# Optimization experiments

Hardware: AMD Instinct MI355X
Metric: run time of the kernel (lower is better)

Reference implementation:

```python
import jax, jax.numpy as jnp
import numpy as np

B, BT = 64, 16              # total crops, true batch (B = 4 crops * BT)
IMG, PATCH, C = 224, 16, 3
EMB, HEADS, DEPTH = 192, 3, 12
MLP = 4 * EMB
NPATCH = (IMG // PATCH) ** 2      # 196
NTOK = NPATCH + 1                 # 197 (cls + patches)
NSLICE = 16
SAT_H, SAT_DK = 8, 32             # ScaledDotProductAttention(d_model=192, d_k=d_v=32, h=8)
SAT_D = SAT_H * SAT_DK            # 256


def setup_inputs() -> dict:
    ks = jax.random.split(jax.random.key(0), 16)
    n = lambda i, shape: jax.random.normal(ks[i], shape, jnp.float32) * 0.02
    z = lambda *s: jnp.zeros(s, jnp.float32)
    o = lambda *s: jnp.ones(s, jnp.float32)
    return {
        "x": jax.random.normal(ks[0], (B, C, IMG, IMG), jnp.float32),
        "x_g_norm": jax.random.uniform(ks[1], (BT, 1, IMG, IMG), dtype=jnp.float32),
        "per_li": jnp.linspace(1.0 / 16.0, 15.0 / 16.0, 15, dtype=jnp.float32),
        "per_li_var": jnp.linspace(0.01, 0.15, 15, dtype=jnp.float32),
        "patch_w": n(2, (EMB, C, PATCH, PATCH)), "patch_b": z(EMB),
        "cls_token": n(3, (1, 1, EMB)), "pos_embed": n(4, (1, NTOK, EMB)),
        "eleva_embed": n(5, (NSLICE, EMB)), "eleva_var_embed": n(6, (NSLICE, EMB)),
        "sat_wq": n(7, (EMB, SAT_D)), "sat_bq": z(SAT_D),
        "sat_wk": n(8, (EMB, SAT_D)), "sat_bk": z(SAT_D),
        "sat_wv": n(9, (EMB, SAT_D)), "sat_bv": z(SAT_D),
        "sat_wo": n(10, (SAT_D, EMB)), "sat_bo": z(EMB),
        "ln1_w": o(DEPTH, EMB), "ln1_b": z(DEPTH, EMB),
        "qkv_w": n(11, (DEPTH, EMB, 3 * EMB)),
        "proj_w": n(12, (DEPTH, EMB, EMB)), "proj_b": z(DEPTH, EMB),
        "ln2_w": o(DEPTH, EMB), "ln2_b": z(DEPTH, EMB),
        "fc1_w": n(13, (DEPTH, EMB, MLP)), "fc1_b": z(DEPTH, MLP),
        "fc2_w": n(14, (DEPTH, MLP, EMB)), "fc2_b": z(DEPTH, EMB),
        "lnf_w": o(EMB), "lnf_b": z(EMB),
    }


def _ln(x, w, b, eps=1e-5):
    mu = x.mean(-1, keepdims=True)
    var = ((x - mu) ** 2).mean(-1, keepdims=True)
    return (x - mu) * jax.lax.rsqrt(var + eps) * w + b


def reference(x, x_g_norm, per_li, per_li_var, patch_w, patch_b, cls_token, pos_embed,
              eleva_embed, eleva_var_embed, sat_wq, sat_bq, sat_wk, sat_bk, sat_wv, sat_bv,
              sat_wo, sat_bo, ln1_w, ln1_b, qkv_w, proj_w, proj_b, ln2_w, ln2_b,
              fc1_w, fc1_b, fc2_w, fc2_b, lnf_w, lnf_b):
    Btot, Bt = x.shape[0], x_g_norm.shape[0]
    # --- PatchEmbed (Conv2d patch=stride=16) ---
    feat = jax.lax.conv_general_dilated(
        x, patch_w, (PATCH, PATCH), 'VALID',
        dimension_numbers=('NCHW', 'OIHW', 'NCHW')) + patch_b[None, :, None, None]
    tok = feat.reshape(Btot, EMB, NPATCH).transpose(0, 2, 1)          # [B,196,E]
    tok = jnp.concatenate([jnp.broadcast_to(cls_token, (Btot, 1, EMB)), tok], 1)
    tok = tok + pos_embed                                             # [B,197,E]
    # --- elevation indices (bisect_left on per-sample mean / unbiased var) ---
    flat = x_g_norm.reshape(Bt, -1)
    idx = jnp.searchsorted(per_li, flat.mean(-1), side='left')
    vidx = jnp.searchsorted(per_li_var, jnp.var(flat, axis=-1, ddof=1), side='left')
    crops = Btot // Bt
    ele = jnp.tile(eleva_embed[idx], (crops, 1))                      # [B,E]
    vele = jnp.tile(eleva_var_embed[vidx], (crops, 1))                # [B,E]
    # --- tiny 3-token attention per (sample, token), batched ---
    at = jnp.stack([tok,
                    jnp.broadcast_to(ele[:, None, :], tok.shape),
                    jnp.broadcast_to(vele[:, None, :], tok.shape)], axis=2)  # [B,T,3,E]
    M = Btot * NTOK
    at = at.reshape(M, 3, EMB)
    q = (at @ sat_wq + sat_bq).reshape(M, 3, SAT_H, SAT_DK).transpose(0, 2, 1, 3)
    k = (at @ sat_wk + sat_bk).reshape(M, 3, SAT_H, SAT_DK).transpose(0, 2, 1, 3)
    v = (at @ sat_wv + sat_bv).reshape(M, 3, SAT_H, SAT_DK).transpose(0, 2, 1, 3)
    att = jax.nn.softmax(jnp.einsum('mhqd,mhkd->mhqk', q, k) / np.sqrt(SAT_DK).astype(np.float32), axis=-1)
    o = jnp.einsum('mhqk,mhkd->mhqd', att, v).transpose(0, 2, 1, 3).reshape(M, 3, SAT_D)
    o = o @ sat_wo + sat_bo                                           # [M,3,E]
    tok = o.sum(1).reshape(Btot, NTOK, EMB)   # token' + eleEm' + elevarEm'
    # --- standard ViT blocks ---
    hd = EMB // HEADS
    scale = hd ** -0.5
    for i in range(DEPTH):
        h = _ln(tok, ln1_w[i], ln1_b[i])
        qkv = (h @ qkv_w[i]).reshape(Btot, NTOK, 3, HEADS, hd).transpose(2, 0, 3, 1, 4)
        a = jax.nn.softmax(jnp.einsum('bhqd,bhkd->bhqk', qkv[0], qkv[1]) * scale, axis=-1)
        h = jnp.einsum('bhqk,bhkd->bhqd', a, qkv[2]).transpose(0, 2, 1, 3).reshape(Btot, NTOK, EMB)
        tok = tok + h @ proj_w[i] + proj_b[i]
        h2 = _ln(tok, ln2_w[i], ln2_b[i])
        h2 = jax.nn.gelu(h2 @ fc1_w[i] + fc1_b[i], approximate=False)
        tok = tok + h2 @ fc2_w[i] + fc2_b[i]
    tok = _ln(tok, lnf_w, lnf_b)
    return tok[:, 0]
```

## Files before the change

### kernel.cpp

```cpp
#include <hip/hip_runtime.h>
#include <hip/hip_bf16.h>
#include <math.h>

#define NB 64
#define NBT 16
#define IMG 224
#define CIN 3
#define EMB 192
#define NHEADS 3
#define DEPTH 12
#define MLPD (4*EMB)
#define NPATCH 196
#define NTOK 197
#define M_TOK (NB*NTOK)
#define M_PATCH (NB*NPATCH)
#define SAT_H 8
#define SAT_DK 32
#define SAT_D 256
#define KPV 232

typedef __attribute__((ext_vector_type(8))) short bf16x8;
typedef __attribute__((ext_vector_type(4))) float f32x4;
typedef __hip_bfloat16 bf16;

__device__ __forceinline__ float bf2f(ushort u) { return __uint_as_float(((unsigned)u) << 16); }
__device__ __forceinline__ ushort f2bf(float f) {
    bf16 h = __float2bfloat16(f);
    return *reinterpret_cast<ushort*>(&h);
}

__global__ __launch_bounds__(256) void stats1_kernel(const float* __restrict__ xg, double* __restrict__ part)
{
    int j = blockIdx.x, s = blockIdx.y;
    const float4* src = (const float4*)(xg + (size_t)s*(IMG*IMG)) + (size_t)j*784;
    double ls = 0.0, lq = 0.0;
    for (int i = threadIdx.x; i < 784; i += 256) {
        float4 v = src[i];
        double a = v.x, b = v.y, c = v.z, d = v.w;
        ls += a+b+c+d;
        lq += a*a + b*b + c*c + d*d;
    }
    __shared__ double ssum[256], ssq[256];
    ssum[threadIdx.x] = ls; ssq[threadIdx.x] = lq;
    __syncthreads();
    for (int st = 128; st > 0; st >>= 1) {
        if (threadIdx.x < st) { ssum[threadIdx.x] += ssum[threadIdx.x+st]; ssq[threadIdx.x] += ssq[threadIdx.x+st]; }
        __syncthreads();
    }
    if (threadIdx.x == 0) {
        part[(size_t)(s*16 + j)*2]     = ssum[0];
        part[(size_t)(s*16 + j)*2 + 1] = ssq[0];
    }
}

__global__ __launch_bounds__(64) void stats2_kernel(const double* __restrict__ part,
    const float* __restrict__ per_li, const float* __restrict__ per_li_var, int* __restrict__ idx_out)
{
    int s = blockIdx.x;
    if (threadIdx.x != 0) return;
    double sum = 0.0, sq = 0.0;
    for (int j = 0; j < 16; j++) { sum += part[(size_t)(s*16+j)*2]; sq += part[(size_t)(s*16+j)*2+1]; }
    double n = (double)(IMG*IMG);
    double mean = sum / n;
    double var  = (sq - n*mean*mean) / (n - 1.0);
    int i1 = 0, i2 = 0;
    for (int j = 0; j < 15; j++) {
        if ((double)per_li[j] < mean) i1++;
        if ((double)per_li_var[j] < var) i2++;
    }
    idx_out[s] = i1; idx_out[16 + s] = i2;
}

__global__ __launch_bounds__(256) void transpose_cast_kernel(const float* __restrict__ in,
    bf16* __restrict__ out, int K, int N)
{
    in  += (size_t)blockIdx.z*K*N;
    out += (size_t)blockIdx.z*N*K;
    __shared__ float t[32][33];
    int k0 = blockIdx.y*32, n0 = blockIdx.x*32;
    int tx = threadIdx.x & 31, ty = threadIdx.x >> 5;
    #pragma unroll
    for (int i = 0; i < 4; i++) {
        int k = ty + i*8;
        t[k][tx] = in[(size_t)(k0+k)*N + n0 + tx];
    }
    __syncthreads();
    #pragma unroll
    for (int i = 0; i < 4; i++) {
        int n = ty + i*8;
        out[(size_t)(n0+n)*K + k0 + tx] = __float2bfloat16(t[tx][n]);
    }
}

__global__ __launch_bounds__(256) void cast_kernel(const float* __restrict__ in, bf16* __restrict__ out, int n)
{
    int i = blockIdx.x*256 + threadIdx.x;
    if (i < n) out[i] = __float2bfloat16(in[i]);
}

__global__ __launch_bounds__(256) void concat3_kernel(const float* __restrict__ a,
    const float* __restrict__ b, const float* __restrict__ c, float* __restrict__ o)
{
    int i = blockIdx.x*256 + threadIdx.x;
    if (i < 256) o[i] = a[i];
    else if (i < 512) o[i] = b[i-256];
    else if (i < 768) o[i] = c[i-512];
}

__global__ __launch_bounds__(256) void im2col_kernel(const float* __restrict__ x, bf16* __restrict__ out)
{
    int e = blockIdx.x*256 + threadIdx.x;
    if (e >= M_PATCH*768) return;
    int row = e / 768, col = e % 768;
    int b = row / NPATCH, p = row % NPATCH;
    int py = p / 14, px = p % 14;
    int c = col >> 8, r8 = col & 255;
    int i = r8 >> 4, j = r8 & 15;
    out[e] = __float2bfloat16(x[(((size_t)b*CIN + c)*IMG + py*16 + i)*IMG + px*16 + j]);
}

__global__ void cls_kernel(const float* __restrict__ cls, const float* __restrict__ pos, bf16* __restrict__ tokb)
{
    int i = blockIdx.x*256 + threadIdx.x;
    if (i >= NB*EMB) return;
    int b = i / EMB, e = i % EMB;
    tokb[(size_t)(b*NTOK)*EMB + e] = __float2bfloat16(cls[e] + pos[e]);
}

template<int EPI, bool OBF>
__global__ __launch_bounds__(256) void mfma_gemm(
    const bf16* __restrict__ A, const bf16* __restrict__ Wt,
    const float* __restrict__ bias, const float* __restrict__ aux,
    void* __restrict__ Cv, int M, int N, int K, int ldc, float bias_scale)
{
    __shared__ bf16 As[64][72];
    __shared__ bf16 Bs[64][72];
    int tid = threadIdx.x;
    int wave = tid >> 6, lane = tid & 63;
    int wm = wave >> 1, wn = wave & 1;
    int m0 = blockIdx.y*64, n0 = blockIdx.x*64;
    f32x4 acc[2][2] = {};
    int sr = tid >> 3, sc = (tid & 7) * 8;

    for (int k0 = 0; k0 < K; k0 += 64) {
        #pragma unroll
        for (int it = 0; it < 2; it++) {
            int r = sr + it*32;
            *(uint4*)&As[r][sc] = *(const uint4*)(A  + (size_t)(m0 + r)*K + k0 + sc);
            *(uint4*)&Bs[r][sc] = *(const uint4*)(Wt + (size_t)(n0 + r)*K + k0 + sc);
        }
        __syncthreads();
        #pragma unroll
        for (int ks = 0; ks < 2; ks++) {
            int ko = ks*32 + (lane >> 4)*8;
            bf16x8 af[2], bfr[2];
            #pragma unroll
            for (int mi = 0; mi < 2; mi++) af[mi]  = *(const bf16x8*)&As[wm*32 + mi*16 + (lane & 15)][ko];
            #pragma unroll
            for (int ni = 0; ni < 2; ni++) bfr[ni] = *(const bf16x8*)&Bs[wn*32 + ni*16 + (lane & 15)][ko];
            #pragma unroll
            for (int mi = 0; mi < 2; mi++)
                #pragma unroll
                for (int ni = 0; ni < 2; ni++)
                    acc[mi][ni] = __builtin_amdgcn_mfma_f32_16x16x32_bf16(af[mi], bfr[ni], acc[mi][ni], 0, 0, 0);
        }
        __syncthreads();
    }
    #pragma unroll
    for (int mi = 0; mi < 2; mi++) {
        #pragma unroll
        for (int ni = 0; ni < 2; ni++) {
            int rbase = m0 + wm*32 + mi*16 + (lane >> 4)*4;
            int col   = n0 + wn*32 + ni*16 + (lane & 15);
            #pragma unroll
            for (int r = 0; r < 4; r++) {
                int row = rbase + r;
                float v = acc[mi][ni][r];
                if constexpr (EPI == 4) {
                    int b_ = row / NPATCH, p = row % NPATCH;
                    ((bf16*)Cv)[(size_t)(b_*NTOK + 1 + p)*EMB + col] =
                        __float2bfloat16(v + bias[col] + aux[(size_t)(1+p)*EMB + col]);
                } else if constexpr (EPI == 5) {
                    int hd = row >> 6, d = row & 63;
                    int bb = col / NTOK, t = col - bb*NTOK;
                    ((bf16*)Cv)[((size_t)((bb*3 + hd)*64 + d))*KPV + t] = __float2bfloat16(v);
                } else {
                    if constexpr (EPI == 1) v += bias[col]*bias_scale;
                    if constexpr (EPI == 2) v = ((float*)Cv)[(size_t)row*ldc + col] + v + bias[col];
                    if constexpr (EPI == 3) { v += bias[col]; v = 0.5f*v*(1.0f + erff(v*0.70710678118654752f)); }
                    if constexpr (OBF) ((bf16*)Cv)[(size_t)row*ldc + col] = __float2bfloat16(v);
                    else               ((float*)Cv)[(size_t)row*ldc + col] = v;
                }
            }
        }
    }
}

template<bool RESID>
__global__ __launch_bounds__(256) void mfma_gemm_ln(
    const bf16* __restrict__ A, const bf16* __restrict__ Wt,
    const float* __restrict__ bias, float bias_scale,
    const float* __restrict__ lnw, const float* __restrict__ lnb,
    float* __restrict__ tokf, bf16* __restrict__ hbB, int K)
{
    __shared__ bf16 As[16][72];
    __shared__ bf16 Bs[192][72];
    __shared__ float sB[192], sW[192], sLb[192];
    __shared__ float redS[4][16], redQ[4][16];
    int tid = threadIdx.x;
    int m0 = blockIdx.x*16;
    int wave = tid >> 6, lane = tid & 63;
    int qc = lane & 15, g = lane >> 4;
    if (tid < 192) { sB[tid] = bias[tid]*bias_scale; sW[tid] = lnw[tid]; sLb[tid] = lnb[tid]; }
    f32x4 acc[3] = {};
    int sr = tid >> 3, sc = (tid & 7)*8;

    for (int k0 = 0; k0 < K; k0 += 64) {
        if (tid < 128) {
            int r = tid >> 3, c = (tid & 7)*8;
            *(uint4*)&As[r][c] = *(const uint4*)(A + (size_t)(m0 + r)*K + k0 + c);
        }
        #pragma unroll
        for (int it = 0; it < 6; it++)
            *(uint4*)&Bs[sr + it*32][sc] = *(const uint4*)(Wt + (size_t)(sr + it*32)*K + k0 + sc);
        __syncthreads();
        #pragma unroll
        for (int ks = 0; ks < 2; ks++) {
            bf16x8 af = *(const bf16x8*)&As[qc][ks*32 + g*8];
            #pragma unroll
            for (int c = 0; c < 3; c++) {
                bf16x8 bf_ = *(const bf16x8*)&Bs[wave*48 + c*16 + qc][ks*32 + g*8];
                acc[c] = __builtin_amdgcn_mfma_f32_16x16x32_bf16(af, bf_, acc[c], 0, 0, 0);
            }
        }
        __syncthreads();
    }
    float v[3][4];
    #pragma unroll
    for (int c = 0; c < 3; c++) {
        int col = wave*48 + c*16 + qc;
        #pragma unroll
        for (int r = 0; r < 4; r++) {
            float t = acc[c][r] + sB[col];
            if constexpr (RESID) t += tokf[(size_t)(m0 + 4*g + r)*EMB + col];
            v[c][r] = t;
        }
    }
    #pragma unroll
    for (int r = 0; r < 4; r++) {
        float s = v[0][r] + v[1][r] + v[2][r];
        #pragma unroll
        for (int o = 1; o < 16; o <<= 1) s += __shfl_xor(s, o);
        if (qc == 0) redS[wave][4*g + r] = s;
    }
    __syncthreads();
    float mu[4];
    #pragma unroll
    for (int r = 0; r < 4; r++) {
        int m = 4*g + r;
        mu[r] = (redS[0][m] + redS[1][m] + redS[2][m] + redS[3][m]) * (1.0f/EMB);
    }
    #pragma unroll
    for (int r = 0; r < 4; r++) {
        float d0 = v[0][r]-mu[r], d1 = v[1][r]-mu[r], d2 = v[2][r]-mu[r];
        float q = d0*d0 + d1*d1 + d2*d2;
        #pragma unroll
        for (int o = 1; o < 16; o <<= 1) q += __shfl_xor(q, o);
        if (qc == 0) redQ[wave][4*g + r] = q;
    }
    __syncthreads();
    float rstd[4];
    #pragma unroll
    for (int r = 0; r < 4; r++) {
        int m = 4*g + r;
        float q = redQ[0][m] + redQ[1][m] + redQ[2][m] + redQ[3][m];
        rstd[r] = rsqrtf(q*(1.0f/EMB) + 1e-5f);
    }
    #pragma unroll
    for (int c = 0; c < 3; c++) {
        int col = wave*48 + c*16 + qc;
        #pragma unroll
        for (int r = 0; r < 4; r++) {
            size_t idx = (size_t)(m0 + 4*g + r)*EMB + col;
            tokf[idx] = v[c][r];
            hbB[idx] = __float2bfloat16((v[c][r]-mu[r])*rstd[r]*sW[col] + sLb[col]);
        }
    }
}

__global__ __launch_bounds__(256) void sat_rows_kernel(
    const float* __restrict__ eleva, const float* __restrict__ eleva_var,
    const float* __restrict__ wq, const float* __restrict__ bq,
    const float* __restrict__ wk, const float* __restrict__ bk,
    const float* __restrict__ wv, const float* __restrict__ bv,
    const int* __restrict__ idx, float* __restrict__ proj, float* __restrict__ sconst)
{
    int s = blockIdx.x;
    __shared__ float ev[2][EMB];
    __shared__ float pr[6][SAT_D];
    int t = threadIdx.x;
    for (int i = t; i < 2*EMB; i += 256) {
        if (i < EMB) ev[0][i] = eleva[(size_t)idx[s]*EMB + i];
        else         ev[1][i-EMB] = eleva_var[(size_t)idx[16+s]*EMB + (i-EMB)];
    }
    __syncthreads();
    for (int j = 0; j < 6; j++) {
        const float* vec = ev[(j >= 3) ? 1 : 0];
        const float* Wm = (j%3 == 0) ? wq : ((j%3 == 1) ? wk : wv);
        const float* bm = (j%3 == 0) ? bq : ((j%3 == 1) ? bk : bv);
        float accv = bm[t];
        for (int k = 0; k < EMB; k++) accv += vec[k]*Wm[(size_t)k*SAT_D + t];
        pr[j][t] = accv;
        proj[((size_t)s*6 + j)*SAT_D + t] = accv;
    }
    __syncthreads();
    if (t < 32) {
        int h = t >> 2, c = t & 3;
        const float* qv = pr[(c < 2) ? 0 : 3];
        const float* kv = pr[((c & 1) == 0) ? 1 : 4];
        float d = 0.f;
        for (int x = 0; x < SAT_DK; x++) d += qv[h*32+x]*kv[h*32+x];
        sconst[((size_t)s*8 + h)*4 + c] = d * 0.17677669529663687f;
    }
}

__global__ __launch_bounds__(256) void sat_attn_kernel(
    const bf16* __restrict__ qkv0, const float* __restrict__ proj,
    const float* __restrict__ sconst, bf16* __restrict__ osum)
{
    int b = blockIdx.x;
    int s = b & 15;
    __shared__ float pr[6][SAT_D];
    __shared__ float sc[8][4];
    for (int i = threadIdx.x; i < 6*SAT_D; i += 256) pr[i >> 8][i & 255] = proj[(size_t)s*6*SAT_D + i];
    if (threadIdx.x < 32) sc[threadIdx.x >> 2][threadIdx.x & 3] = sconst[(size_t)s*32 + threadIdx.x];
    __syncthreads();
    int t = threadIdx.x;
    if (t >= NTOK) return;
    size_t m = (size_t)b*NTOK + t;
    const ushort* q0 = (const ushort*)(qkv0 + m*768);
    const ushort* k0 = q0 + 256;
    const ushort* v0 = q0 + 512;
    const float inv = 0.17677669529663687f;
    for (int h = 0; h < SAT_H; h++) {
        int d0 = h*32;
        float S00=0,S01=0,S02=0,S10=0,S20=0;
        #pragma unroll 8
        for (int d = 0; d < 32; d++) {
            float qv = bf2f(q0[d0+d]), kv = bf2f(k0[d0+d]);
            S00 += qv*kv;
            S01 += qv*pr[1][d0+d];
            S02 += qv*pr[4][d0+d];
            S10 += pr[0][d0+d]*kv;
            S20 += pr[3][d0+d]*kv;
        }
        S00*=inv; S01*=inv; S02*=inv; S10*=inv; S20*=inv;
        float al=0.f, be=0.f, ga=0.f;
        {
            float mx = fmaxf(S00, fmaxf(S01, S02));
            float e0 = expf(S00-mx), e1 = expf(S01-mx), e2 = expf(S02-mx);
            float is = 1.0f/(e0+e1+e2); al += e0*is; be += e1*is; ga += e2*is;
        }
        {
            float a1 = sc[h][0], a2 = sc[h][1];
            float mx = fmaxf(S10, fmaxf(a1, a2));
            float e0 = expf(S10-mx), e1 = expf(a1-mx), e2 = expf(a2-mx);
            float is = 1.0f/(e0+e1+e2); al += e0*is; be += e1*is; ga += e2*is;
        }
        {
            float a1 = sc[h][2], a2 = sc[h][3];
            float mx = fmaxf(S20, fmaxf(a1, a2));
            float e0 = expf(S20-mx), e1 = expf(a1-mx), e2 = expf(a2-mx);
            float is = 1.0f/(e0+e1+e2); al += e0*is; be += e1*is; ga += e2*is;
        }
        #pragma unroll 8
        for (int d = 0; d < 32; d++)
            osum[m*SAT_D + d0 + d] = __float2bfloat16(al*bf2f(v0[d0+d]) + be*pr[2][d0+d] + ga*pr[5][d0+d]);
    }
}

__global__ __launch_bounds__(256) void vit_attn_mfma(
    const bf16* __restrict__ qkv, const bf16* __restrict__ vT, bf16* __restrict__ hout)
{
    __shared__ ushort Ks[208*72];
    __shared__ ushort Vt[64*KPV];
    __shared__ ushort Pl[4][16*KPV];

    int u = (blockIdx.x & 7)*96 + (blockIdx.x >> 3);
    int qg = u & 3, hd = (u >> 2) % 3, b = u / 12;
    int tid = threadIdx.x;
    size_t rowQ = (size_t)b*NTOK;

    for (int i = tid; i < 208*8; i += 256) {
        int k = i >> 3, c = i & 7;
        uint4 v = make_uint4(0u,0u,0u,0u);
        if (k < NTOK) v = *(const uint4*)(qkv + (rowQ + k)*384 + 192 + hd*64 + c*8);
        *(uint4*)&Ks[(size_t)k*72 + c*8] = v;
    }
    {
        const uint4* vsrc = (const uint4*)(vT + (size_t)((b*3 + hd)*64)*KPV);
        uint4* vdst = (uint4*)Vt;
        for (int i = tid; i < 64*KPV/8; i += 256) vdst[i] = vsrc[i];
    }
    __syncthreads();

    int wave = tid >> 6, lane = tid & 63;
    int qstart = (13*qg + 3) >> 2;
    int qcnt   = ((13*(qg+1) + 3) >> 2) - qstart;
    if (wave >= qcnt) return;
    int q0 = (qstart + wave)*16;
    int qcol = lane & 15, g = lane >> 4;

    bf16x8 qf[2] = {};
    if (q0 + qcol < NTOK) {
        const bf16* qp = qkv + (rowQ + q0 + qcol)*384 + hd*64 + g*8;
        qf[0] = *(const bf16x8*)qp;
        qf[1] = *(const bf16x8*)(qp + 32);
    }

    f32x4 st[13] = {};
    #pragma unroll
    for (int t = 0; t < 13; t++) {
        const ushort* krow = &Ks[(size_t)(16*t + qcol)*72];
        bf16x8 a0 = *(const bf16x8*)(krow + g*8);
        bf16x8 a1 = *(const bf16x8*)(krow + 32 + g*8);
        st[t] = __builtin_amdgcn_mfma_f32_16x16x32_bf16(a0, qf[0], st[t], 0, 0, 0);
        st[t] = __builtin_amdgcn_mfma_f32_16x16x32_bf16(a1, qf[1], st[t], 0, 0, 0);
    }

    const float scale = 0.125f;
    float mx = -1e30f;
    #pragma unroll
    for (int t = 0; t < 13; t++)
        #pragma unroll
        for (int r = 0; r < 4; r++) {
            int key = 16*t + 4*g + r;
            float s = st[t][r]*scale;
            st[t][r] = s;
            if (key < NTOK) mx = fmaxf(mx, s);
        }
    mx = fmaxf(mx, __shfl_xor(mx, 16));
    mx = fmaxf(mx, __shfl_xor(mx, 32));
    float sum = 0.f;
    #pragma unroll
    for (int t = 0; t < 13; t++)
        #pragma unroll
        for (int r = 0; r < 4; r++) {
            int key = 16*t + 4*g + r;
            float e = (key < NTOK) ? __expf(st[t][r] - mx) : 0.f;
            st[t][r] = e; sum += e;
        }
    sum += __shfl_xor(sum, 16);
    sum += __shfl_xor(sum, 32);
    float isv = 1.f/sum;

    ushort* P = Pl[wave];
    #pragma unroll
    for (int t = 0; t < 13; t++)
        #pragma unroll
        for (int r = 0; r < 4; r++)
            P[(size_t)qcol*KPV + 16*t + 4*g + r] = f2bf(st[t][r]*isv);
    #pragma unroll
    for (int r = 0; r < 4; r++)
        P[(size_t)qcol*KPV + 208 + 4*g + r] = 0;

    f32x4 oacc[4] = {};
    #pragma unroll
    for (int ks = 0; ks < 7; ks++) {
        bf16x8 pf = *(const bf16x8*)&P[(size_t)qcol*KPV + ks*32 + g*8];
        #pragma unroll
        for (int dt = 0; dt < 4; dt++) {
            bf16x8 vf = *(const bf16x8*)&Vt[(size_t)(dt*16 + qcol)*KPV + ks*32 + g*8];
            oacc[dt] = __builtin_amdgcn_mfma_f32_16x16x32_bf16(pf, vf, oacc[dt], 0, 0, 0);
        }
    }

    int nq = NTOK - q0; if (nq > 16) nq = 16;
    #pragma unroll
    for (int dt = 0; dt < 4; dt++)
        #pragma unroll
        for (int r = 0; r < 4; r++) {
            int q = 4*g + r;
            if (q < nq)
                hout[(rowQ + q0 + q)*EMB + hd*64 + dt*16 + qcol] = __float2bfloat16(oacc[dt][r]);
        }
}

__global__ __launch_bounds__(64) void final_ln_kernel(const float* __restrict__ tok,
    const float* __restrict__ w, const float* __restrict__ b_, float* __restrict__ out)
{
    int b = blockIdx.x, lane = threadIdx.x;
    const float* x = tok + (size_t)b*NTOK*EMB;
    float x0 = x[lane], x1 = x[lane+64], x2 = x[lane+128];
    float s = x0+x1+x2;
    for (int o = 32; o > 0; o >>= 1) s += __shfl_xor(s, o);
    float mu = s * (1.0f/EMB);
    float d0 = x0-mu, d1 = x1-mu, d2 = x2-mu;
    float ss = d0*d0 + d1*d1 + d2*d2;
    for (int o = 32; o > 0; o >>= 1) ss += __shfl_xor(ss, o);
    float rs = rsqrtf(ss*(1.0f/EMB) + 1e-5f);
    out[(size_t)b*EMB + lane]     = d0*rs*w[lane]     + b_[lane];
    out[(size_t)b*EMB + lane+64]  = d1*rs*w[lane+64]  + b_[lane+64];
    out[(size_t)b*EMB + lane+128] = d2*rs*w[lane+128] + b_[lane+128];
}

extern "C" void kernel_launch(void* const* d_in, const int* in_sizes, int n_in,
                              void* d_out, int out_size, void* d_ws, size_t ws_size,
                              hipStream_t stream)
{
    const float* x          = (const float*)d_in[0];
    const float* xg         = (const float*)d_in[1];
    const float* per_li     = (const float*)d_in[2];
    const float* per_li_var = (const float*)d_in[3];
    const float* patch_w    = (const float*)d_in[4];
    const float* patch_b    = (const float*)d_in[5];
    const float* cls_token  = (const float*)d_in[6];
    const float* pos_embed  = (const float*)d_in[7];
    const float* eleva      = (const float*)d_in[8];
    const float* eleva_var  = (const float*)d_in[9];
    const float* sat_wq     = (const float*)d_in[10];
    const float* sat_bq     = (const float*)d_in[11];
    const float* sat_wk     = (const float*)d_in[12];
    const float* sat_bk     = (const float*)d_in[13];
    const float* sat_wv     = (const float*)d_in[14];
    const float* sat_bv     = (const float*)d_in[15];
    const float* sat_wo     = (const float*)d_in[16];
    const float* sat_bo     = (const float*)d_in[17];
    const float* ln1_w      = (const float*)d_in[18];
    const float* ln1_b      = (const float*)d_in[19];
    const float* qkv_w      = (const float*)d_in[20];
    const float* proj_w     = (const float*)d_in[21];
    const float* proj_b     = (const float*)d_in[22];
    const float* ln2_w      = (const float*)d_in[23];
    const float* ln2_b      = (const float*)d_in[24];
    const float* fc1_w      = (const float*)d_in[25];
    const float* fc1_b      = (const float*)d_in[26];
    const float* fc2_w      = (const float*)d_in[27];
    const float* fc2_b      = (const float*)d_in[28];
    const float* lnf_w      = (const float*)d_in[29];
    const float* lnf_b      = (const float*)d_in[30];
    float* out = (float*)d_out;

    char* p = (char*)d_ws;
    float* tokf = (float*)p;                 p += (size_t)M_TOK*EMB*4;
    bf16* hb    = (bf16*)p;                  p += (size_t)M_TOK*EMB*2;
    bf16* tokb  = (bf16*)p;                  p += (size_t)M_TOK*EMB*2;
    bf16* qkvb  = (bf16*)p;                  p += (size_t)M_TOK*768*2;
    bf16* osum  = (bf16*)p;                  p += (size_t)M_TOK*SAT_D*2;
    bf16* vTb   = (bf16*)p;                  p += (size_t)NB*3*64*KPV*2;
    bf16* qkv_wt  = (bf16*)p;                p += (size_t)DEPTH*576*EMB*2;
    bf16* proj_wt = (bf16*)p;                p += (size_t)DEPTH*EMB*EMB*2;
    bf16* fc1_wt  = (bf16*)p;                p += (size_t)DEPTH*MLPD*EMB*2;
    bf16* fc2_wt  = (bf16*)p;                p += (size_t)DEPTH*EMB*MLPD*2;
    bf16* patch_wb= (bf16*)p;                p += (size_t)EMB*768*2;
    bf16* sat_wqkvt = (bf16*)p;              p += (size_t)3*SAT_D*EMB*2;
    bf16* sat_wot = (bf16*)p;                p += (size_t)EMB*SAT_D*2;
    float* sat_bqkv = (float*)p;             p += 768*4;
    float* projb  = (float*)p;               p += 16*6*SAT_D*4;
    float* sconst = (float*)p;               p += 16*32*4;
    double* statp = (double*)p;              p += 256*2*8;
    int*   idxb   = (int*)p;

    transpose_cast_kernel<<<dim3(576/32, EMB/32, DEPTH), 256, 0, stream>>>(qkv_w,  qkv_wt,  EMB, 576);
    transpose_cast_kernel<<<dim3(EMB/32, EMB/32, DEPTH), 256, 0, stream>>>(proj_w, proj_wt, EMB, EMB);
    transpose_cast_kernel<<<dim3(MLPD/32, EMB/32, DEPTH), 256, 0, stream>>>(fc1_w, fc1_wt,  EMB, MLPD);
    transpose_cast_kernel<<<dim3(EMB/32, MLPD/32, DEPTH), 256, 0, stream>>>(fc2_w, fc2_wt,  MLPD, EMB);
    transpose_cast_kernel<<<dim3(SAT_D/32, EMB/32, 1), 256, 0, stream>>>(sat_wq, sat_wqkvt,              EMB, SAT_D);
    transpose_cast_kernel<<<dim3(SAT_D/32, EMB/32, 1), 256, 0, stream>>>(sat_wk, sat_wqkvt + 256*EMB,    EMB, SAT_D);
    transpose_cast_kernel<<<dim3(SAT_D/32, EMB/32, 1), 256, 0, stream>>>(sat_wv, sat_wqkvt + 512*EMB,    EMB, SAT_D);
    transpose_cast_kernel<<<dim3(EMB/32, SAT_D/32, 1), 256, 0, stream>>>(sat_wo, sat_wot, SAT_D, EMB);
    concat3_kernel<<<3, 256, 0, stream>>>(sat_bq, sat_bk, sat_bv, sat_bqkv);
    cast_kernel<<<(EMB*768 + 255)/256, 256, 0, stream>>>(patch_w, patch_wb, EMB*768);

    stats1_kernel<<<dim3(16, 16), 256, 0, stream>>>(xg, statp);
    stats2_kernel<<<16, 64, 0, stream>>>(statp, per_li, per_li_var, idxb);
    im2col_kernel<<<(M_PATCH*768 + 255)/256, 256, 0, stream>>>(x, qkvb);
    mfma_gemm<4,true><<<dim3(EMB/64, M_PATCH/64), 256, 0, stream>>>(
        qkvb, patch_wb, patch_b, pos_embed, tokb, M_PATCH, EMB, 768, EMB, 1.0f);
    cls_kernel<<<(NB*EMB + 255)/256, 256, 0, stream>>>(cls_token, pos_embed, tokb);
    sat_rows_kernel<<<16, 256, 0, stream>>>(eleva, eleva_var, sat_wq, sat_bq, sat_wk, sat_bk,
                                            sat_wv, sat_bv, idxb, projb, sconst);
    mfma_gemm<1,true><<<dim3(768/64, M_TOK/64), 256, 0, stream>>>(
        tokb, sat_wqkvt, sat_bqkv, nullptr, qkvb, M_TOK, 768, EMB, 768, 1.0f);
    sat_attn_kernel<<<NB, 256, 0, stream>>>(qkvb, projb, sconst, osum);
    mfma_gemm_ln<false><<<M_TOK/16, 256, 0, stream>>>(
        osum, sat_wot, sat_bo, 3.0f, ln1_w, ln1_b, tokf, hb, SAT_D);
    for (int i = 0; i < DEPTH; i++) {
        mfma_gemm<0,true><<<dim3(384/64, M_TOK/64), 256, 0, stream>>>(
            hb, qkv_wt + (size_t)i*576*EMB, nullptr, nullptr, qkvb, M_TOK, 384, EMB, 384, 1.0f);
        mfma_gemm<5,true><<<dim3(M_TOK/64, EMB/64), 256, 0, stream>>>(
            qkv_wt + ((size_t)i*576 + 384)*EMB, hb, nullptr, nullptr, vTb, EMB, M_TOK, EMB, 0, 1.0f);
        vit_attn_mfma<<<768, 256, 0, stream>>>(qkvb, vTb, hb);
        mfma_gemm_ln<true><<<M_TOK/16, 256, 0, stream>>>(
            hb, proj_wt + (size_t)i*EMB*EMB, proj_b + i*EMB, 1.0f,
            ln2_w + i*EMB, ln2_b + i*EMB, tokf, hb, EMB);
        mfma_gemm<3,true><<<dim3(MLPD/64, M_TOK/64), 256, 0, stream>>>(
            hb, fc1_wt + (size_t)i*MLPD*EMB, fc1_b + i*MLPD, nullptr, qkvb, M_TOK, MLPD, EMB, MLPD, 1.0f);
        if (i < DEPTH-1) {
            mfma_gemm_ln<true><<<M_TOK/16, 256, 0, stream>>>(
                qkvb, fc2_wt + (size_t)i*EMB*MLPD, fc2_b + i*EMB, 1.0f,
                ln1_w + (i+1)*EMB, ln1_b + (i+1)*EMB, tokf, hb, MLPD);
        } else {
            mfma_gemm<2,false><<<dim3(EMB/64, M_TOK/64), 256, 0, stream>>>(
                qkvb, fc2_wt + (size_t)i*EMB*MLPD, fc2_b + i*EMB, nullptr, tokf, M_TOK, EMB, MLPD, EMB, 1.0f);
        }
    }
    final_ln_kernel<<<NB, 64, 0, stream>>>(tokf, lnf_w, lnf_b, out);
}
```

Baseline: 1.383 ms.

## Merge weight transposes and QKV GEMMs into single launches, stage 3 K-chunks per sync

The eight weight transpose launches become one flat-grid kernel that picks its source by block index. The per-layer Q/K GEMM and the transposed V GEMM are merged into a single launch with 1773 blocks, so both run concurrently and launch count drops. The generic GEMM gets a template parameter that loads three 64-wide K chunks per barrier, cutting sync count but tripling LDS use (about 55KB per block), which may reduce occupancy.

```diff
diff --git a/kernel.cpp b/kernel.cpp
--- a/kernel.cpp
+++ b/kernel.cpp
@@ -71,25 +71,34 @@
     idx_out[s] = i1; idx_out[16 + s] = i2;
 }
 
-__global__ __launch_bounds__(256) void transpose_cast_kernel(const float* __restrict__ in,
-    bf16* __restrict__ out, int K, int N)
-{
-    in  += (size_t)blockIdx.z*K*N;
-    out += (size_t)blockIdx.z*N*K;
+__global__ __launch_bounds__(256) void prep_transpose_kernel(
+    const float* __restrict__ qkv_w, const float* __restrict__ proj_w,
+    const float* __restrict__ fc1_w, const float* __restrict__ fc2_w,
+    const float* __restrict__ swq, const float* __restrict__ swk,
+    const float* __restrict__ swv, const float* __restrict__ swo,
+    bf16* __restrict__ qkv_wt, bf16* __restrict__ proj_wt,
+    bf16* __restrict__ fc1_wt, bf16* __restrict__ fc2_wt,
+    bf16* __restrict__ sat_wqkvt, bf16* __restrict__ sat_wot)
+{
+    int id = blockIdx.x;
+    const float* in; bf16* outp; int K, N, r;
+    if (id < 1296)      { int z = id/108,       rr = id%108; in = qkv_w  + (size_t)z*192*576; outp = qkv_wt  + (size_t)z*576*192; K=192; N=576; r = rr; }
+    else if (id < 1728) { int z = (id-1296)/36, rr = (id-1296)%36; in = proj_w + (size_t)z*192*192; outp = proj_wt + (size_t)z*192*192; K=192; N=192; r = rr; }
+    else if (id < 3456) { int z = (id-1728)/144, rr = (id-1728)%144; in = fc1_w + (size_t)z*192*768; outp = fc1_wt + (size_t)z*768*192; K=192; N=768; r = rr; }
+    else if (id < 5184) { int z = (id-3456)/144, rr = (id-3456)%144; in = fc2_w + (size_t)z*768*192; outp = fc2_wt + (size_t)z*192*768; K=768; N=192; r = rr; }
+    else if (id < 5232) { in = swq; outp = sat_wqkvt;            K=192; N=256; r = id-5184; }
+    else if (id < 5280) { in = swk; outp = sat_wqkvt + 256*192;  K=192; N=256; r = id-5232; }
+    else if (id < 5328) { in = swv; outp = sat_wqkvt + 512*192;  K=192; N=256; r = id-5280; }
+    else                { in = swo; outp = sat_wot;              K=256; N=192; r = id-5328; }
+    int nbx = N/32;
+    int k0 = (r/nbx)*32, n0 = (r%nbx)*32;
     __shared__ float t[32][33];
-    int k0 = blockIdx.y*32, n0 = blockIdx.x*32;
     int tx = threadIdx.x & 31, ty = threadIdx.x >> 5;
     #pragma unroll
-    for (int i = 0; i < 4; i++) {
-        int k = ty + i*8;
-        t[k][tx] = in[(size_t)(k0+k)*N + n0 + tx];
-    }
-    __syncthreads();
-    #pragma unroll
-    for (int i = 0; i < 4; i++) {
-        int n = ty + i*8;
-        out[(size_t)(n0+n)*K + k0 + tx] = __float2bfloat16(t[tx][n]);
-    }
+    for (int i = 0; i < 4; i++) t[ty + i*8][tx] = in[(size_t)(k0 + ty + i*8)*N + n0 + tx];
+    __syncthreads();
+    #pragma unroll
+    for (int i = 0; i < 4; i++) outp[(size_t)(n0 + ty + i*8)*K + k0 + tx] = __float2bfloat16(t[tx][ty + i*8]);
 }
 
 __global__ __launch_bounds__(256) void cast_kernel(const float* __restrict__ in, bf16* __restrict__ out, int n)
@@ -127,14 +136,14 @@
     tokb[(size_t)(b*NTOK)*EMB + e] = __float2bfloat16(cls[e] + pos[e]);
 }
 
-template<int EPI, bool OBF>
+template<int EPI, bool OBF, int BKC>
 __global__ __launch_bounds__(256) void mfma_gemm(
     const bf16* __restrict__ A, const bf16* __restrict__ Wt,
     const float* __restrict__ bias, const float* __restrict__ aux,
     void* __restrict__ Cv, int M, int N, int K, int ldc, float bias_scale)
 {
-    __shared__ bf16 As[64][72];
-    __shared__ bf16 Bs[64][72];
+    __shared__ bf16 As[BKC][64][72];
+    __shared__ bf16 Bs[BKC][64][72];
     int tid = threadIdx.x;
     int wave = tid >> 6, lane = tid & 63;
     int wm = wave >> 1, wn = wave & 1;
@@ -142,27 +151,33 @@
     f32x4 acc[2][2] = {};
     int sr = tid >> 3, sc = (tid & 7) * 8;
 
-    for (int k0 = 0; k0 < K; k0 += 64) {
-        #pragma unroll
-        for (int it = 0; it < 2; it++) {
-            int r = sr + it*32;
-            *(uint4*)&As[r][sc] = *(const uint4*)(A  + (size_t)(m0 + r)*K + k0 + sc);
-            *(uint4*)&Bs[r][sc] = *(const uint4*)(Wt + (size_t)(n0 + r)*K + k0 + sc);
+    for (int k0 = 0; k0 < K; k0 += BKC*64) {
+        #pragma unroll
+        for (int c = 0; c < BKC; c++) {
+            #pragma unroll
+            for (int it = 0; it < 2; it++) {
+                int r = sr + it*32;
+                *(uint4*)&As[c][r][sc] = *(const uint4*)(A  + (size_t)(m0 + r)*K + k0 + c*64 + sc);
+                *(uint4*)&Bs[c][r][sc] = *(const uint4*)(Wt + (size_t)(n0 + r)*K + k0 + c*64 + sc);
+            }
         }
         __syncthreads();
         #pragma unroll
-        for (int ks = 0; ks < 2; ks++) {
-            int ko = ks*32 + (lane >> 4)*8;
-            bf16x8 af[2], bfr[2];
-            #pragma unroll
-            for (int mi = 0; mi < 2; mi++) af[mi]  = *(const bf16x8*)&As[wm*32 + mi*16 + (lane & 15)][ko];
-            #pragma unroll
-            for (int ni = 0; ni < 2; ni++) bfr[ni] = *(const bf16x8*)&Bs[wn*32 + ni*16 + (lane & 15)][ko];
-            #pragma unroll
-            for (int mi = 0; mi < 2; mi++)
+        for (int c = 0; c < BKC; c++) {
+            #pragma unroll
+            for (int ks = 0; ks < 2; ks++) {
+                int ko = ks*32 + (lane >> 4)*8;
+                bf16x8 af[2], bfr[2];
                 #pragma unroll
-                for (int ni = 0; ni < 2; ni++)
-                    acc[mi][ni] = __builtin_amdgcn_mfma_f32_16x16x32_bf16(af[mi], bfr[ni], acc[mi][ni], 0, 0, 0);
+                for (int mi = 0; mi < 2; mi++) af[mi]  = *(const bf16x8*)&As[c][wm*32 + mi*16 + (lane & 15)][ko];
+                #pragma unroll
+                for (int ni = 0; ni < 2; ni++) bfr[ni] = *(const bf16x8*)&Bs[c][wn*32 + ni*16 + (lane & 15)][ko];
+                #pragma unroll
+                for (int mi = 0; mi < 2; mi++)
+                    #pragma unroll
+                    for (int ni = 0; ni < 2; ni++)
+                        acc[mi][ni] = __builtin_amdgcn_mfma_f32_16x16x32_bf16(af[mi], bfr[ni], acc[mi][ni], 0, 0, 0);
+            }
         }
         __syncthreads();
     }
@@ -180,10 +195,6 @@
                     int b_ = row / NPATCH, p = row % NPATCH;
                     ((bf16*)Cv)[(size_t)(b_*NTOK + 1 + p)*EMB + col] =
                         __float2bfloat16(v + bias[col] + aux[(size_t)(1+p)*EMB + col]);
-                } else if constexpr (EPI == 5) {
-                    int hd = row >> 6, d = row & 63;
-                    int bb = col / NTOK, t = col - bb*NTOK;
-                    ((bf16*)Cv)[((size_t)((bb*3 + hd)*64 + d))*KPV + t] = __float2bfloat16(v);
                 } else {
                     if constexpr (EPI == 1) v += bias[col]*bias_scale;
                     if constexpr (EPI == 2) v = ((float*)Cv)[(size_t)row*ldc + col] + v + bias[col];
@@ -194,6 +205,68 @@
             }
         }
     }
+}
+
+__global__ __launch_bounds__(256) void qkv_proj_kernel(
+    const bf16* __restrict__ hb, const bf16* __restrict__ wqk,
+    const bf16* __restrict__ wv, bf16* __restrict__ qkvb, bf16* __restrict__ vTb)
+{
+    __shared__ bf16 As[3][64][72];
+    __shared__ bf16 Bs[3][64][72];
+    int id = blockIdx.x;
+    bool isQK = id < 1182;
+    const bf16 *Ap, *Bp; int m0, n0;
+    if (isQK) { int bx = id % 6,  by = id / 6;          m0 = by*64; n0 = bx*64; Ap = hb; Bp = wqk; }
+    else      { int id2 = id - 1182; int bx = id2 % 197, by = id2 / 197; m0 = by*64; n0 = bx*64; Ap = wv; Bp = hb; }
+    int tid = threadIdx.x;
+    int wave = tid >> 6, lane = tid & 63;
+    int wm = wave >> 1, wn = wave & 1;
+    f32x4 acc[2][2] = {};
+    int sr = tid >> 3, sc = (tid & 7)*8;
+    #pragma unroll
+    for (int c = 0; c < 3; c++)
+        #pragma unroll
+        for (int it = 0; it < 2; it++) {
+            int r = sr + it*32;
+            *(uint4*)&As[c][r][sc] = *(const uint4*)(Ap + (size_t)(m0 + r)*192 + c*64 + sc);
+            *(uint4*)&Bs[c][r][sc] = *(const uint4*)(Bp + (size_t)(n0 + r)*192 + c*64 + sc);
+        }
+    __syncthreads();
+    #pragma unroll
+    for (int c = 0; c < 3; c++)
+        #pragma unroll
+        for (int ks = 0; ks < 2; ks++) {
+            int ko = ks*32 + (lane >> 4)*8;
+            bf16x8 af[2], bfr[2];
+            #pragma unroll
+            for (int mi = 0; mi < 2; mi++) af[mi]  = *(const bf16x8*)&As[c][wm*32 + mi*16 + (lane & 15)][ko];
+            #pragma unroll
+            for (int ni = 0; ni < 2; ni++) bfr[ni] = *(const bf16x8*)&Bs[c][wn*32 + ni*16 + (lane & 15)][ko];
+            #pragma unroll
+            for (int mi = 0; mi < 2; mi++)
+                #pragma unroll
+                for (int ni = 0; ni < 2; ni++)
+                    acc[mi][ni] = __builtin_amdgcn_mfma_f32_16x16x32_bf16(af[mi], bfr[ni], acc[mi][ni], 0, 0, 0);
+        }
+    #pragma unroll
+    for (int mi = 0; mi < 2; mi++)
+        #pragma unroll
+        for (int ni = 0; ni < 2; ni++) {
+            int rbase = m0 + wm*32 + mi*16 + (lane >> 4)*4;
+            int col   = n0 + wn*32 + ni*16 + (lane & 15);
+            #pragma unroll
+            for (int r = 0; r < 4; r++) {
+                int row = rbase + r;
+                float v = acc[mi][ni][r];
+                if (isQK) {
+                    qkvb[(size_t)row*384 + col] = __float2bfloat16(v);
+                } else {
+                    int hd = row >> 6, d = row & 63;
+                    int bb = col / NTOK, t = col - bb*NTOK;
+                    vTb[((size_t)((bb*3 + hd)*64 + d))*KPV + t] = __float2bfloat16(v);
+                }
+            }
+        }
 }
 
 template<bool RESID>
@@ -561,47 +634,40 @@
     double* statp = (double*)p;              p += 256*2*8;
     int*   idxb   = (int*)p;
 
-    transpose_cast_kernel<<<dim3(576/32, EMB/32, DEPTH), 256, 0, stream>>>(qkv_w,  qkv_wt,  EMB, 576);
-    transpose_cast_kernel<<<dim3(EMB/32, EMB/32, DEPTH), 256, 0, stream>>>(proj_w, proj_wt, EMB, EMB);
-    transpose_cast_kernel<<<dim3(MLPD/32, EMB/32, DEPTH), 256, 0, stream>>>(fc1_w, fc1_wt,  EMB, MLPD);
-    transpose_cast_kernel<<<dim3(EMB/32, MLPD/32, DEPTH), 256, 0, stream>>>(fc2_w, fc2_wt,  MLPD, EMB);
-    transpose_cast_kernel<<<dim3(SAT_D/32, EMB/32, 1), 256, 0, stream>>>(sat_wq, sat_wqkvt,              EMB, SAT_D);
-    transpose_cast_kernel<<<dim3(SAT_D/32, EMB/32, 1), 256, 0, stream>>>(sat_wk, sat_wqkvt + 256*EMB,    EMB, SAT_D);
-    transpose_cast_kernel<<<dim3(SAT_D/32, EMB/32, 1), 256, 0, stream>>>(sat_wv, sat_wqkvt + 512*EMB,    EMB, SAT_D);
-    transpose_cast_kernel<<<dim3(EMB/32, SAT_D/32, 1), 256, 0, stream>>>(sat_wo, sat_wot, SAT_D, EMB);
+    prep_transpose_kernel<<<5376, 256, 0, stream>>>(
+        qkv_w, proj_w, fc1_w, fc2_w, sat_wq, sat_wk, sat_wv, sat_wo,
+        qkv_wt, proj_wt, fc1_wt, fc2_wt, sat_wqkvt, sat_wot);
     concat3_kernel<<<3, 256, 0, stream>>>(sat_bq, sat_bk, sat_bv, sat_bqkv);
     cast_kernel<<<(EMB*768 + 255)/256, 256, 0, stream>>>(patch_w, patch_wb, EMB*768);
 
     stats1_kernel<<<dim3(16, 16), 256, 0, stream>>>(xg, statp);
     stats2_kernel<<<16, 64, 0, stream>>>(statp, per_li, per_li_var, idxb);
     im2col_kernel<<<(M_PATCH*768 + 255)/256, 256, 0, stream>>>(x, qkvb);
-    mfma_gemm<4,true><<<dim3(EMB/64, M_PATCH/64), 256, 0, stream>>>(
+    mfma_gemm<4,true,3><<<dim3(EMB/64, M_PATCH/64), 256, 0, stream>>>(
         qkvb, patch_wb, patch_b, pos_embed, tokb, M_PATCH, EMB, 768, EMB, 1.0f);
     cls_kernel<<<(NB*EMB + 255)/256, 256, 0, stream>>>(cls_token, pos_embed, tokb);
     sat_rows_kernel<<<16, 256, 0, stream>>>(eleva, eleva_var, sat_wq, sat_bq, sat_wk, sat_bk,
                                             sat_wv, sat_bv, idxb, projb, sconst);
-    mfma_gemm<1,true><<<dim3(768/64, M_TOK/64), 256, 0, stream>>>(
+    mfma_gemm<1,true,3><<<dim3(768/64, M_TOK/64), 256, 0, stream>>>(
         tokb, sat_wqkvt, sat_bqkv, nullptr, qkvb, M_TOK, 768, EMB, 768, 1.0f);
     sat_attn_kernel<<<NB, 256, 0, stream>>>(qkvb, projb, sconst, osum);
     mfma_gemm_ln<false><<<M_TOK/16, 256, 0, stream>>>(
         osum, sat_wot, sat_bo, 3.0f, ln1_w, ln1_b, tokf, hb, SAT_D);
     for (int i = 0; i < DEPTH; i++) {
-        mfma_gemm<0,true><<<dim3(384/64, M_TOK/64), 256, 0, stream>>>(
-            hb, qkv_wt + (size_t)i*576*EMB, nullptr, nullptr, qkvb, M_TOK, 384, EMB, 384, 1.0f);
-        mfma_gemm<5,true><<<dim3(M_TOK/64, EMB/64), 256, 0, stream>>>(
-            qkv_wt + ((size_t)i*576 + 384)*EMB, hb, nullptr, nullptr, vTb, EMB, M_TOK, EMB, 0, 1.0f);
+        qkv_proj_kernel<<<1773, 256, 0, stream>>>(
+            hb, qkv_wt + (size_t)i*576*EMB, qkv_wt + ((size_t)i*576 + 384)*EMB, qkvb, vTb);
         vit_attn_mfma<<<768, 256, 0, stream>>>(qkvb, vTb, hb);
         mfma_gemm_ln<true><<<M_TOK/16, 256, 0, stream>>>(
             hb, proj_wt + (size_t)i*EMB*EMB, proj_b + i*EMB, 1.0f,
             ln2_w + i*EMB, ln2_b + i*EMB, tokf, hb, EMB);
-        mfma_gemm<3,true><<<dim3(MLPD/64, M_TOK/64), 256, 0, stream>>>(
+        mfma_gemm<3,true,3><<<dim3(MLPD/64, M_TOK/64), 256, 0, stream>>>(
             hb, fc1_wt + (size_t)i*MLPD*EMB, fc1_b + i*MLPD, nullptr, qkvb, M_TOK, MLPD, EMB, MLPD, 1.0f);
         if (i < DEPTH-1) {
             mfma_gemm_ln<true><<<M_TOK/16, 256, 0, stream>>>(
                 qkvb, fc2_wt + (size_t)i*EMB*MLPD, fc2_b + i*EMB, 1.0f,
                 ln1_w + (i+1)*EMB, ln1_b + (i+1)*EMB, tokf, hb, MLPD);
         } else {
-            mfma_gemm<2,false><<<dim3(EMB/64, M_TOK/64), 256, 0, stream>>>(
+            mfma_gemm<2,false,3><<<dim3(EMB/64, M_TOK/64), 256, 0, stream>>>(
                 qkvb, fc2_wt + (size_t)i*EMB*MLPD, fc2_b + i*EMB, nullptr, tokf, M_TOK, EMB, MLPD, EMB, 1.0f);
         }
     }
```

New measurement: 1.353 ms. -2.2%, faster.
